# Optimization experiments

Hardware: AMD Instinct MI355X
Metric: run time of the kernel (lower is better)

Reference implementation:

```python
import jax, jax.numpy as jnp
import numpy as np

N_DRUG, N_DIS, E, D = 10000, 15000, 1048576, 128

def setup_inputs() -> dict:
    key = jax.random.key(0)
    k = jax.random.split(key, 6)
    return {
        "z_drug": jax.random.normal(k[0], (N_DRUG, D), dtype=jnp.float32),
        "z_disease": jax.random.normal(k[1], (N_DIS, D), dtype=jnp.float32),
        "row": jax.random.randint(k[2], (E,), 0, N_DRUG),
        "col": jax.random.randint(k[3], (E,), 0, N_DIS),
        "W1": jax.random.normal(k[4], (2 * D, D), dtype=jnp.float32) * (1.0 / np.sqrt(2 * D)),
        "b1": jnp.zeros((D,), dtype=jnp.float32),
        "W2": jax.random.normal(k[5], (D, 1), dtype=jnp.float32) * (1.0 / np.sqrt(D)),
        "b2": jnp.zeros((1,), dtype=jnp.float32),
    }

def reference(z_drug, z_disease, row, col, W1, b1, W2, b2):
    # gather per-edge embeddings and concatenate: [E, 2D]
    z = jnp.concatenate([z_drug[row], z_disease[col]], axis=-1)
    h = jax.nn.relu(z @ W1 + b1)          # [E, D]
    out = h @ W2 + b2                      # [E, 1]
    return out.reshape(-1)                 # [E]
```

## Files before the change

kernel.cpp:

```cpp
#include <hip/hip_runtime.h>

typedef __attribute__((ext_vector_type(8))) short short8;
typedef __attribute__((ext_vector_type(4))) float floatx4;
typedef _Float16 half8 __attribute__((ext_vector_type(8)));
typedef _Float16 half4 __attribute__((ext_vector_type(4)));
typedef _Float16 half2v __attribute__((ext_vector_type(2)));

static __device__ __forceinline__ unsigned short f2bf(float x) {
    unsigned int u = __builtin_bit_cast(unsigned int, x);
    unsigned int r = (u + 0x7FFFu + ((u >> 16) & 1u)) >> 16;
    return (unsigned short)r;
}

__global__ __launch_bounds__(256, 2) void mid_kernel(
    const float* __restrict__ zd, const float* __restrict__ zs,
    const float* __restrict__ W1, const float* __restrict__ b1,
    _Float16* __restrict__ ud, _Float16* __restrict__ us,
    int ndrows, int nsrows, int ntd, int nbg,
    const int* __restrict__ row, const int* __restrict__ col,
    unsigned* __restrict__ gcur, unsigned long long* __restrict__ recbuf, int E)
{
    if ((int)blockIdx.x < nbg) {
        const int tid  = threadIdx.x;
        const int lane = tid & 63;
        const int wave = tid >> 6;
        const int wh   = wave >> 1;
        const int we   = wave & 1;
        const int l15  = lane & 15;
        const int quad = lane >> 4;

        const int b = blockIdx.x;
        const bool isD = (b < ntd);
        const float* __restrict__ z = isD ? zd : zs;
        _Float16* __restrict__ u = isD ? ud : us;
        const int nrows = isD ? ndrows : nsrows;
        const int m0    = (isD ? b : b - ntd) * 64;
        const int koff0 = isD ? 0 : 128;
        const int whbase = wh * 64;

        short8 wfrag[16];
        #pragma unroll
        for (int s = 0; s < 4; ++s)
            #pragma unroll
            for (int mt = 0; mt < 4; ++mt) {
                short8 t;
                #pragma unroll
                for (int j = 0; j < 8; ++j)
                    t[j] = (short)f2bf(
                        W1[(size_t)(koff0 + s * 32 + quad * 8 + j) * 128 +
                           whbase + mt * 16 + l15]);
                wfrag[s * 4 + mt] = t;
            }

        floatx4 acc[2][4];
        #pragma unroll
        for (int mt = 0; mt < 4; ++mt) {
            floatx4 bb = *reinterpret_cast<const floatx4*>(&b1[whbase + mt * 16 + quad * 4]);
            bb *= 0.5f;
            acc[0][mt] = bb;
            acc[1][mt] = bb;
        }

        int rowi[2], rowc[2];
        #pragma unroll
        for (int et = 0; et < 2; ++et) {
            rowi[et] = m0 + we * 32 + et * 16 + l15;
            rowc[et] = rowi[et] < nrows ? rowi[et] : nrows - 1;
        }

        #pragma unroll
        for (int s = 0; s < 4; ++s) {
            short8 bf[2];
            #pragma unroll
            for (int et = 0; et < 2; ++et) {
                const float* src = &z[(size_t)rowc[et] * 128 + s * 32 + quad * 8];
                floatx4 lo = *reinterpret_cast<const floatx4*>(src);
                floatx4 hi = *reinterpret_cast<const floatx4*>(src + 4);
                short8 t;
                t[0] = (short)f2bf(lo[0]); t[1] = (short)f2bf(lo[1]);
                t[2] = (short)f2bf(lo[2]); t[3] = (short)f2bf(lo[3]);
                t[4] = (short)f2bf(hi[0]); t[5] = (short)f2bf(hi[1]);
                t[6] = (short)f2bf(hi[2]); t[7] = (short)f2bf(hi[3]);
                bf[et] = t;
            }
            #pragma unroll
            for (int et = 0; et < 2; ++et)
                #pragma unroll
                for (int mt = 0; mt < 4; ++mt)
                    acc[et][mt] = __builtin_amdgcn_mfma_f32_16x16x32_bf16(
                        wfrag[s * 4 + mt], bf[et], acc[et][mt], 0, 0, 0);
        }

        #pragma unroll
        for (int et = 0; et < 2; ++et) {
            if (rowi[et] < nrows) {
                #pragma unroll
                for (int mt = 0; mt < 4; ++mt) {
                    half4 hv;
                    #pragma unroll
                    for (int rr = 0; rr < 4; ++rr) hv[rr] = (_Float16)acc[et][mt][rr];
                    *reinterpret_cast<half4*>(
                        &u[(size_t)rowi[et] * 128 + whbase + mt * 16 + quad * 4]) = hv;
                }
            }
        }
    } else {
        __shared__ unsigned wl[4][4];
        __shared__ unsigned gb[4];
        const int tid  = threadIdx.x;
        const int lane = tid & 63;
        const int wave = tid >> 6;
        const int sb   = blockIdx.x - nbg;
        const long base = (long)sb * 2048;

        unsigned rc[8], off[8];
        int cls0, cls1, cls2, cls3, cls4, cls5, cls6, cls7;
        unsigned w0 = 0, w1 = 0, w2c = 0, w3 = 0;

        #pragma unroll
        for (int k = 0; k < 8; ++k) {
            long e = base + wave * 512 + k * 64 + lane;
            int r = row[e], c = col[e];
            rc[k] = (unsigned)r | ((unsigned)c << 14);
            int cl = ((r >= 5000) ? 2 : 0) | ((c >= 7500) ? 1 : 0);
            unsigned long long m0 = __ballot(cl == 0);
            unsigned long long m1 = __ballot(cl == 1);
            unsigned long long m2 = __ballot(cl == 2);
            unsigned long long m3 = __ballot(cl == 3);
            unsigned long long mlt = (1ull << lane) - 1ull;
            unsigned long long mc = (cl == 0) ? m0 : (cl == 1) ? m1 : (cl == 2) ? m2 : m3;
            unsigned wb = (cl == 0) ? w0 : (cl == 1) ? w1 : (cl == 2) ? w2c : w3;
            off[k] = wb + (unsigned)__popcll(mc & mlt);
            w0 += (unsigned)__popcll(m0); w1 += (unsigned)__popcll(m1);
            w2c += (unsigned)__popcll(m2); w3 += (unsigned)__popcll(m3);
            switch (k) {
                case 0: cls0 = cl; break; case 1: cls1 = cl; break;
                case 2: cls2 = cl; break; case 3: cls3 = cl; break;
                case 4: cls4 = cl; break; case 5: cls5 = cl; break;
                case 6: cls6 = cl; break; default: cls7 = cl; break;
            }
        }
        if (lane < 4) {
            unsigned wv = (lane == 0) ? w0 : (lane == 1) ? w1 : (lane == 2) ? w2c : w3;
            wl[wave][lane] = wv;
        }
        __syncthreads();
        if (tid < 4) {
            unsigned tot = wl[0][tid] + wl[1][tid] + wl[2][tid] + wl[3][tid];
            gb[tid] = atomicAdd(&gcur[tid], tot);
        }
        __syncthreads();
        unsigned p0 = 0, p1 = 0, p2 = 0, p3 = 0;
        for (int w = 0; w < 4; ++w)
            if (w < wave) { p0 += wl[w][0]; p1 += wl[w][1]; p2 += wl[w][2]; p3 += wl[w][3]; }

        #pragma unroll
        for (int k = 0; k < 8; ++k) {
            long e = base + wave * 512 + k * 64 + lane;
            int cl = (k == 0) ? cls0 : (k == 1) ? cls1 : (k == 2) ? cls2 : (k == 3) ? cls3
                   : (k == 4) ? cls4 : (k == 5) ? cls5 : (k == 6) ? cls6 : cls7;
            unsigned pre = (cl == 0) ? p0 : (cl == 1) ? p1 : (cl == 2) ? p2 : p3;
            unsigned pos = gb[cl] + pre + off[k];
            recbuf[(size_t)cl * E + pos] =
                (unsigned long long)rc[k] | ((unsigned long long)(unsigned)e << 32);
        }
    }
}

__global__ __launch_bounds__(256, 6) void edge_eval(
    const _Float16* __restrict__ ud, const _Float16* __restrict__ us,
    const unsigned* __restrict__ gcur, const unsigned long long* __restrict__ recbuf,
    const float* __restrict__ w2, const float* __restrict__ b2,
    float* __restrict__ out, int E)
{
    const int tid  = threadIdx.x;
    const int lane = tid & 63;
    const int wave = tid >> 6;
    const int le   = lane >> 3;
    const int q    = lane & 7;
    const int lslot = wave * 8 + le;

    const int b    = blockIdx.x;
    const int cls  = (b & 7) >> 1;
    const int sub  = ((b >> 3) << 1) | (b & 1);
    const int NSUB = (int)((gridDim.x >> 3) << 1);

    const unsigned n = gcur[cls];
    const int nch = (int)((n + 31u) >> 5);
    const unsigned long long* __restrict__ recb = recbuf + (size_t)cls * E;

#if __has_builtin(__builtin_amdgcn_fdot2)
    half2v w2h[8];
    #pragma unroll
    for (int i = 0; i < 2; ++i)
        #pragma unroll
        for (int p = 0; p < 4; ++p) {
            half2v t;
            t[0] = (_Float16)w2[i * 64 + q * 8 + 2 * p];
            t[1] = (_Float16)w2[i * 64 + q * 8 + 2 * p + 1];
            w2h[i * 4 + p] = t;
        }
#else
    float w2r[16];
    #pragma unroll
    for (int i = 0; i < 2; ++i) {
        *reinterpret_cast<floatx4*>(&w2r[i * 8]) =
            *reinterpret_cast<const floatx4*>(&w2[i * 64 + q * 8]);
        *reinterpret_cast<floatx4*>(&w2r[i * 8 + 4]) =
            *reinterpret_cast<const floatx4*>(&w2[i * 64 + q * 8 + 4]);
    }
#endif
    const float b2v = b2[0];

    const int K = (nch + NSUB - 1) / NSUB;
    int t = sub * K;
    int tend = t + K;
    if (tend > nch) tend = nch;
    if (t >= tend) return;

#define LOADREC(RV, VV, tt)                                                    \
    {                                                                          \
        unsigned ei = (unsigned)(tt) * 32u + (unsigned)lslot;                  \
        VV = ei < n;                                                           \
        RV = recb[VV ? ei : 0u];                                               \
    }

#define GATHER(D, RV)                                                          \
    {                                                                          \
        unsigned r = (unsigned)(RV) & 16383u;                                  \
        unsigned c = ((unsigned)(RV) >> 14) & 16383u;                          \
        const _Float16* up = ud + (size_t)r * 128 + q * 8;                     \
        const _Float16* vp = us + (size_t)c * 128 + q * 8;                     \
        D[0] = *reinterpret_cast<const half8*>(up);                            \
        D[1] = *reinterpret_cast<const half8*>(up + 64);                       \
        D[2] = *reinterpret_cast<const half8*>(vp);                            \
        D[3] = *reinterpret_cast<const half8*>(vp + 64);                       \
    }

#if __has_builtin(__builtin_amdgcn_fdot2)
#define DOTBODY(D, accv)                                                       \
    half8 s0 = D[0] + D[2];                                                    \
    s0 = __builtin_elementwise_max(s0, (half8)(_Float16)0.f);                  \
    half8 s1 = D[1] + D[3];                                                    \
    s1 = __builtin_elementwise_max(s1, (half8)(_Float16)0.f);                  \
    _Pragma("unroll")                                                          \
    for (int p = 0; p < 4; ++p) {                                              \
        half2v pr0; pr0[0] = s0[2 * p]; pr0[1] = s0[2 * p + 1];                \
        accv = __builtin_amdgcn_fdot2(pr0, w2h[p], accv, false);               \
        half2v pr1; pr1[0] = s1[2 * p]; pr1[1] = s1[2 * p + 1];                \
        accv = __builtin_amdgcn_fdot2(pr1, w2h[4 + p], accv, false);           \
    }
#else
#define DOTBODY(D, accv)                                                       \
    half8 s0 = D[0] + D[2];                                                    \
    s0 = __builtin_elementwise_max(s0, (half8)(_Float16)0.f);                  \
    half8 s1 = D[1] + D[3];                                                    \
    s1 = __builtin_elementwise_max(s1, (half8)(_Float16)0.f);                  \
    _Pragma("unroll")                                                          \
    for (int j = 0; j < 8; ++j) {                                              \
        accv += (float)s0[j] * w2r[j];                                         \
        accv += (float)s1[j] * w2r[8 + j];                                     \
    }
#endif

#define COMPUTE(D, RV, VV)                                                     \
    {                                                                          \
        float acc = 0.f;                                                       \
        DOTBODY(D, acc)                                                        \
        acc += __shfl_xor(acc, 1);                                             \
        acc += __shfl_xor(acc, 2);                                             \
        acc += __shfl_xor(acc, 4);                                             \
        if ((VV) && q == 0) out[(unsigned)((RV) >> 32)] = acc + b2v;           \
    }

    unsigned long long recA, recB = 0, recA2 = 0, recB2 = 0;
    bool vA, vB = false, vA2 = false, vB2 = false;
    LOADREC(recA, vA, t)
    bool hasB = (t + 1 < tend);
    if (hasB) LOADREC(recB, vB, t + 1)

    half8 dA[4], dB[4];
    while (true) {
        GATHER(dA, recA)
        if (hasB) GATHER(dB, recB)

        bool hasA2 = (t + 2 < tend), hasB2 = (t + 3 < tend);
        if (hasA2) LOADREC(recA2, vA2, t + 2)
        if (hasB2) LOADREC(recB2, vB2, t + 3)

        COMPUTE(dA, recA, vA)
        if (!hasB) break;
        COMPUTE(dB, recB, vB)

        if (!hasA2) break;
        recA = recA2; vA = vA2;
        recB = recB2; vB = vB2;
        hasB = hasB2;
        t += 2;
    }
#undef LOADREC
#undef GATHER
#undef DOTBODY
#undef COMPUTE
}

extern "C" void kernel_launch(void* const* d_in, const int* in_sizes, int n_in,
                              void* d_out, int out_size, void* d_ws, size_t ws_size,
                              hipStream_t stream) {
    const float* zd = (const float*)d_in[0];
    const float* zs = (const float*)d_in[1];
    const int*   row = (const int*)d_in[2];
    const int*   col = (const int*)d_in[3];
    const float* W1 = (const float*)d_in[4];
    const float* b1 = (const float*)d_in[5];
    const float* w2 = (const float*)d_in[6];
    const float* b2 = (const float*)d_in[7];
    float* out = (float*)d_out;

    const int nd = in_sizes[0];
    const int ns = in_sizes[1];
    const int E  = in_sizes[2];
    const int ndrows = nd / 128;
    const int nsrows = ns / 128;

    _Float16* ud = (_Float16*)d_ws;
    _Float16* us = ud + (size_t)ndrows * 128;
    size_t off = (size_t)((char*)(us + (size_t)nsrows * 128) - (char*)d_ws);
    off = (off + 63) & ~(size_t)63;
    unsigned* gcur = (unsigned*)((char*)d_ws + off);
    unsigned long long* recbuf = (unsigned long long*)((char*)gcur + 64);

    hipMemsetAsync(gcur, 0, 16 * sizeof(unsigned), stream);

    const int ntd = (ndrows + 63) / 64;
    const int nts = (nsrows + 63) / 64;
    const int nbg = ntd + nts;
    const int nsb = E / 2048;
    hipLaunchKernelGGL(mid_kernel, dim3(nbg + nsb), dim3(256), 0, stream,
                       zd, zs, W1, b1, ud, us, ndrows, nsrows, ntd, nbg,
                       row, col, gcur, recbuf, E);

    hipLaunchKernelGGL(edge_eval, dim3(1536), dim3(256), 0, stream,
                       ud, us, gcur, recbuf, w2, b2, out, E);
}
```

Before: 123.7 us.

## Replace 4-class edge partition with fine-grained row-bucket counting sort

The old code split edges into four coarse classes by row and column half. The new code builds a histogram over 16-row drug buckets crossed with two column halves, scans it, and scatters each record into a globally sorted order. Edges that share a drug row, or nearby rows, then sit next to each other, which should improve cache reuse of the gathered fp16 rows in the edge kernel. The cost is two more kernel launches (a single-block scan and a scatter pass), a second read of row and col, and local-memory atomics; the edge grid also drops from 1536 to 1024 blocks.

```diff
diff --git a/kernel.cpp b/kernel.cpp
--- a/kernel.cpp
+++ b/kernel.cpp
@@ -12,164 +12,207 @@
     return (unsigned short)r;
 }
 
-__global__ __launch_bounds__(256, 2) void mid_kernel(
+static __device__ void phase_gemm(
+    int b, const float* __restrict__ zd, const float* __restrict__ zs,
+    const float* __restrict__ W1, const float* __restrict__ b1,
+    _Float16* __restrict__ ud, _Float16* __restrict__ us,
+    int ndrows, int nsrows, int ntd)
+{
+    const int tid  = threadIdx.x;
+    const int lane = tid & 63;
+    const int wave = tid >> 6;
+    const int wh   = wave >> 1;
+    const int we   = wave & 1;
+    const int l15  = lane & 15;
+    const int quad = lane >> 4;
+
+    const bool isD = (b < ntd);
+    const float* __restrict__ z = isD ? zd : zs;
+    _Float16* __restrict__ u = isD ? ud : us;
+    const int nrows = isD ? ndrows : nsrows;
+    const int m0    = (isD ? b : b - ntd) * 64;
+    const int koff0 = isD ? 0 : 128;
+    const int whbase = wh * 64;
+
+    short8 wfrag[16];
+    #pragma unroll
+    for (int s = 0; s < 4; ++s)
+        #pragma unroll
+        for (int mt = 0; mt < 4; ++mt) {
+            short8 t;
+            #pragma unroll
+            for (int j = 0; j < 8; ++j)
+                t[j] = (short)f2bf(
+                    W1[(size_t)(koff0 + s * 32 + quad * 8 + j) * 128 +
+                       whbase + mt * 16 + l15]);
+            wfrag[s * 4 + mt] = t;
+        }
+
+    floatx4 acc[2][4];
+    #pragma unroll
+    for (int mt = 0; mt < 4; ++mt) {
+        floatx4 bb = *reinterpret_cast<const floatx4*>(&b1[whbase + mt * 16 + quad * 4]);
+        bb *= 0.5f;
+        acc[0][mt] = bb;
+        acc[1][mt] = bb;
+    }
+
+    int rowi[2], rowc[2];
+    #pragma unroll
+    for (int et = 0; et < 2; ++et) {
+        rowi[et] = m0 + we * 32 + et * 16 + l15;
+        rowc[et] = rowi[et] < nrows ? rowi[et] : nrows - 1;
+    }
+
+    #pragma unroll
+    for (int s = 0; s < 4; ++s) {
+        short8 bf[2];
+        #pragma unroll
+        for (int et = 0; et < 2; ++et) {
+            const float* src = &z[(size_t)rowc[et] * 128 + s * 32 + quad * 8];
+            floatx4 lo = *reinterpret_cast<const floatx4*>(src);
+            floatx4 hi = *reinterpret_cast<const floatx4*>(src + 4);
+            short8 t;
+            t[0] = (short)f2bf(lo[0]); t[1] = (short)f2bf(lo[1]);
+            t[2] = (short)f2bf(lo[2]); t[3] = (short)f2bf(lo[3]);
+            t[4] = (short)f2bf(hi[0]); t[5] = (short)f2bf(hi[1]);
+            t[6] = (short)f2bf(hi[2]); t[7] = (short)f2bf(hi[3]);
+            bf[et] = t;
+        }
+        #pragma unroll
+        for (int et = 0; et < 2; ++et)
+            #pragma unroll
+            for (int mt = 0; mt < 4; ++mt)
+                acc[et][mt] = __builtin_amdgcn_mfma_f32_16x16x32_bf16(
+                    wfrag[s * 4 + mt], bf[et], acc[et][mt], 0, 0, 0);
+    }
+
+    #pragma unroll
+    for (int et = 0; et < 2; ++et) {
+        if (rowi[et] < nrows) {
+            #pragma unroll
+            for (int mt = 0; mt < 4; ++mt) {
+                half4 hv;
+                #pragma unroll
+                for (int rr = 0; rr < 4; ++rr) hv[rr] = (_Float16)acc[et][mt][rr];
+                *reinterpret_cast<half4*>(
+                    &u[(size_t)rowi[et] * 128 + whbase + mt * 16 + quad * 4]) = hv;
+            }
+        }
+    }
+}
+
+static __device__ void phase_hist(
+    int hb, const int* __restrict__ row, const int* __restrict__ col,
+    unsigned* __restrict__ ghist, int E, int nbrow, int colh)
+{
+    __shared__ unsigned lh[1280];
+    const int tid = threadIdx.x;
+    for (int i = tid; i < 1280; i += 256) lh[i] = 0;
+    __syncthreads();
+    const int per = (E + 191) / 192;
+    const int e0 = hb * per;
+    int e1 = e0 + per; if (e1 > E) e1 = E;
+    for (int e = e0 + tid; e < e1; e += 256) {
+        int r = row[e], c = col[e];
+        int bin = ((c >= colh) ? nbrow : 0) + (r >> 4);
+        atomicAdd(&lh[bin], 1u);
+    }
+    __syncthreads();
+    const int nb = 2 * nbrow;
+    for (int i = tid; i < nb; i += 256) {
+        unsigned v = lh[i];
+        if (v) atomicAdd(&ghist[i], v);
+    }
+}
+
+__global__ __launch_bounds__(256, 2) void k_mid(
     const float* __restrict__ zd, const float* __restrict__ zs,
     const float* __restrict__ W1, const float* __restrict__ b1,
     _Float16* __restrict__ ud, _Float16* __restrict__ us,
     int ndrows, int nsrows, int ntd, int nbg,
     const int* __restrict__ row, const int* __restrict__ col,
-    unsigned* __restrict__ gcur, unsigned long long* __restrict__ recbuf, int E)
-{
-    if ((int)blockIdx.x < nbg) {
-        const int tid  = threadIdx.x;
-        const int lane = tid & 63;
-        const int wave = tid >> 6;
-        const int wh   = wave >> 1;
-        const int we   = wave & 1;
-        const int l15  = lane & 15;
-        const int quad = lane >> 4;
-
-        const int b = blockIdx.x;
-        const bool isD = (b < ntd);
-        const float* __restrict__ z = isD ? zd : zs;
-        _Float16* __restrict__ u = isD ? ud : us;
-        const int nrows = isD ? ndrows : nsrows;
-        const int m0    = (isD ? b : b - ntd) * 64;
-        const int koff0 = isD ? 0 : 128;
-        const int whbase = wh * 64;
-
-        short8 wfrag[16];
-        #pragma unroll
-        for (int s = 0; s < 4; ++s)
-            #pragma unroll
-            for (int mt = 0; mt < 4; ++mt) {
-                short8 t;
-                #pragma unroll
-                for (int j = 0; j < 8; ++j)
-                    t[j] = (short)f2bf(
-                        W1[(size_t)(koff0 + s * 32 + quad * 8 + j) * 128 +
-                           whbase + mt * 16 + l15]);
-                wfrag[s * 4 + mt] = t;
-            }
-
-        floatx4 acc[2][4];
-        #pragma unroll
-        for (int mt = 0; mt < 4; ++mt) {
-            floatx4 bb = *reinterpret_cast<const floatx4*>(&b1[whbase + mt * 16 + quad * 4]);
-            bb *= 0.5f;
-            acc[0][mt] = bb;
-            acc[1][mt] = bb;
+    unsigned* __restrict__ ghist, int E, int nbrow, int colh)
+{
+    const int b = blockIdx.x;
+    if (b < nbg) phase_gemm(b, zd, zs, W1, b1, ud, us, ndrows, nsrows, ntd);
+    else         phase_hist(b - nbg, row, col, ghist, E, nbrow, colh);
+}
+
+__global__ void k_scan(const unsigned* __restrict__ ghist, unsigned* __restrict__ gcur,
+                       unsigned* __restrict__ gmeta, int nb, int nbrow)
+{
+    __shared__ unsigned tsum[256];
+    const int tid = threadIdx.x;
+    unsigned v[5];
+    unsigned s = 0;
+    #pragma unroll
+    for (int i = 0; i < 5; ++i) {
+        int idx = tid * 5 + i;
+        v[i] = (idx < nb) ? ghist[idx] : 0u;
+        s += v[i];
+    }
+    tsum[tid] = s;
+    for (int off = 1; off < 256; off <<= 1) {
+        __syncthreads();
+        unsigned y = (tid >= off) ? tsum[tid - off] : 0u;
+        __syncthreads();
+        tsum[tid] += y;
+    }
+    __syncthreads();
+    unsigned running = tsum[tid] - s;
+    #pragma unroll
+    for (int i = 0; i < 5; ++i) {
+        int idx = tid * 5 + i;
+        if (idx < nb) {
+            gcur[idx] = running;
+            if (idx == nbrow) gmeta[0] = running;
+            running += v[i];
         }
-
-        int rowi[2], rowc[2];
-        #pragma unroll
-        for (int et = 0; et < 2; ++et) {
-            rowi[et] = m0 + we * 32 + et * 16 + l15;
-            rowc[et] = rowi[et] < nrows ? rowi[et] : nrows - 1;
-        }
-
-        #pragma unroll
-        for (int s = 0; s < 4; ++s) {
-            short8 bf[2];
-            #pragma unroll
-            for (int et = 0; et < 2; ++et) {
-                const float* src = &z[(size_t)rowc[et] * 128 + s * 32 + quad * 8];
-                floatx4 lo = *reinterpret_cast<const floatx4*>(src);
-                floatx4 hi = *reinterpret_cast<const floatx4*>(src + 4);
-                short8 t;
-                t[0] = (short)f2bf(lo[0]); t[1] = (short)f2bf(lo[1]);
-                t[2] = (short)f2bf(lo[2]); t[3] = (short)f2bf(lo[3]);
-                t[4] = (short)f2bf(hi[0]); t[5] = (short)f2bf(hi[1]);
-                t[6] = (short)f2bf(hi[2]); t[7] = (short)f2bf(hi[3]);
-                bf[et] = t;
-            }
-            #pragma unroll
-            for (int et = 0; et < 2; ++et)
-                #pragma unroll
-                for (int mt = 0; mt < 4; ++mt)
-                    acc[et][mt] = __builtin_amdgcn_mfma_f32_16x16x32_bf16(
-                        wfrag[s * 4 + mt], bf[et], acc[et][mt], 0, 0, 0);
-        }
-
-        #pragma unroll
-        for (int et = 0; et < 2; ++et) {
-            if (rowi[et] < nrows) {
-                #pragma unroll
-                for (int mt = 0; mt < 4; ++mt) {
-                    half4 hv;
-                    #pragma unroll
-                    for (int rr = 0; rr < 4; ++rr) hv[rr] = (_Float16)acc[et][mt][rr];
-                    *reinterpret_cast<half4*>(
-                        &u[(size_t)rowi[et] * 128 + whbase + mt * 16 + quad * 4]) = hv;
-                }
-            }
-        }
-    } else {
-        __shared__ unsigned wl[4][4];
-        __shared__ unsigned gb[4];
-        const int tid  = threadIdx.x;
-        const int lane = tid & 63;
-        const int wave = tid >> 6;
-        const int sb   = blockIdx.x - nbg;
-        const long base = (long)sb * 2048;
-
-        unsigned rc[8], off[8];
-        int cls0, cls1, cls2, cls3, cls4, cls5, cls6, cls7;
-        unsigned w0 = 0, w1 = 0, w2c = 0, w3 = 0;
-
-        #pragma unroll
-        for (int k = 0; k < 8; ++k) {
-            long e = base + wave * 512 + k * 64 + lane;
-            int r = row[e], c = col[e];
-            rc[k] = (unsigned)r | ((unsigned)c << 14);
-            int cl = ((r >= 5000) ? 2 : 0) | ((c >= 7500) ? 1 : 0);
-            unsigned long long m0 = __ballot(cl == 0);
-            unsigned long long m1 = __ballot(cl == 1);
-            unsigned long long m2 = __ballot(cl == 2);
-            unsigned long long m3 = __ballot(cl == 3);
-            unsigned long long mlt = (1ull << lane) - 1ull;
-            unsigned long long mc = (cl == 0) ? m0 : (cl == 1) ? m1 : (cl == 2) ? m2 : m3;
-            unsigned wb = (cl == 0) ? w0 : (cl == 1) ? w1 : (cl == 2) ? w2c : w3;
-            off[k] = wb + (unsigned)__popcll(mc & mlt);
-            w0 += (unsigned)__popcll(m0); w1 += (unsigned)__popcll(m1);
-            w2c += (unsigned)__popcll(m2); w3 += (unsigned)__popcll(m3);
-            switch (k) {
-                case 0: cls0 = cl; break; case 1: cls1 = cl; break;
-                case 2: cls2 = cl; break; case 3: cls3 = cl; break;
-                case 4: cls4 = cl; break; case 5: cls5 = cl; break;
-                case 6: cls6 = cl; break; default: cls7 = cl; break;
-            }
-        }
-        if (lane < 4) {
-            unsigned wv = (lane == 0) ? w0 : (lane == 1) ? w1 : (lane == 2) ? w2c : w3;
-            wl[wave][lane] = wv;
-        }
-        __syncthreads();
-        if (tid < 4) {
-            unsigned tot = wl[0][tid] + wl[1][tid] + wl[2][tid] + wl[3][tid];
-            gb[tid] = atomicAdd(&gcur[tid], tot);
-        }
-        __syncthreads();
-        unsigned p0 = 0, p1 = 0, p2 = 0, p3 = 0;
-        for (int w = 0; w < 4; ++w)
-            if (w < wave) { p0 += wl[w][0]; p1 += wl[w][1]; p2 += wl[w][2]; p3 += wl[w][3]; }
-
-        #pragma unroll
-        for (int k = 0; k < 8; ++k) {
-            long e = base + wave * 512 + k * 64 + lane;
-            int cl = (k == 0) ? cls0 : (k == 1) ? cls1 : (k == 2) ? cls2 : (k == 3) ? cls3
-                   : (k == 4) ? cls4 : (k == 5) ? cls5 : (k == 6) ? cls6 : cls7;
-            unsigned pre = (cl == 0) ? p0 : (cl == 1) ? p1 : (cl == 2) ? p2 : p3;
-            unsigned pos = gb[cl] + pre + off[k];
-            recbuf[(size_t)cl * E + pos] =
-                (unsigned long long)rc[k] | ((unsigned long long)(unsigned)e << 32);
-        }
-    }
-}
-
-__global__ __launch_bounds__(256, 6) void edge_eval(
+    }
+}
+
+__global__ __launch_bounds__(256, 4) void k_scatter(
+    const int* __restrict__ row, const int* __restrict__ col,
+    unsigned* __restrict__ gcur, unsigned long long* __restrict__ recbuf,
+    int E, int nbrow, int colh)
+{
+    __shared__ unsigned lh[1280];
+    const int tid = threadIdx.x;
+    for (int i = tid; i < 1280; i += 256) lh[i] = 0;
+    __syncthreads();
+
+    const int per = E >> 9;
+    const long base = (long)blockIdx.x * per;
+
+    unsigned rnk[8], rcv[8];
+    int binv[8];
+    #pragma unroll
+    for (int k = 0; k < 8; ++k) {
+        long e = base + k * 256 + tid;
+        int r = row[e], c = col[e];
+        rcv[k] = (unsigned)r | ((unsigned)c << 14);
+        binv[k] = ((c >= colh) ? nbrow : 0) + (r >> 4);
+        rnk[k] = atomicAdd(&lh[binv[k]], 1u);
+    }
+    __syncthreads();
+    const int nb = 2 * nbrow;
+    for (int i = tid; i < nb; i += 256) {
+        unsigned cnt = lh[i];
+        if (cnt) lh[i] = atomicAdd(&gcur[i], cnt);
+    }
+    __syncthreads();
+    #pragma unroll
+    for (int k = 0; k < 8; ++k) {
+        long e = base + k * 256 + tid;
+        unsigned pos = lh[binv[k]] + rnk[k];
+        recbuf[pos] = (unsigned long long)rcv[k] | ((unsigned long long)(unsigned)e << 32);
+    }
+}
+
+__global__ __launch_bounds__(256, 4) void k_edge(
     const _Float16* __restrict__ ud, const _Float16* __restrict__ us,
-    const unsigned* __restrict__ gcur, const unsigned long long* __restrict__ recbuf,
+    const unsigned* __restrict__ gmeta, const unsigned long long* __restrict__ recbuf,
     const float* __restrict__ w2, const float* __restrict__ b2,
     float* __restrict__ out, int E)
 {
@@ -180,14 +223,19 @@
     const int q    = lane & 7;
     const int lslot = wave * 8 + le;
 
-    const int b    = blockIdx.x;
-    const int cls  = (b & 7) >> 1;
-    const int sub  = ((b >> 3) << 1) | (b & 1);
-    const int NSUB = (int)((gridDim.x >> 3) << 1);
-
-    const unsigned n = gcur[cls];
-    const int nch = (int)((n + 31u) >> 5);
-    const unsigned long long* __restrict__ recb = recbuf + (size_t)cls * E;
+    const int b   = blockIdx.x;
+    const int cc  = (b & 7) >> 2;
+    const int sub = ((b >> 3) << 2) | (b & 3);
+    const unsigned n0 = gmeta[0];
+    const unsigned c0 = cc ? n0 : 0u;
+    const unsigned nc = cc ? ((unsigned)E - n0) : n0;
+    if (nc == 0) return;
+    const unsigned K = (nc + 511u) >> 9;
+    unsigned start = c0 + (unsigned)sub * K;
+    unsigned climit = c0 + nc;
+    if (start >= climit) return;
+    unsigned end = start + K;
+    if (end > climit) end = climit;
 
 #if __has_builtin(__builtin_amdgcn_fdot2)
     half2v w2h[8];
@@ -211,18 +259,13 @@
     }
 #endif
     const float b2v = b2[0];
-
-    const int K = (nch + NSUB - 1) / NSUB;
-    int t = sub * K;
-    int tend = t + K;
-    if (tend > nch) tend = nch;
-    if (t >= tend) return;
+    const int tend = (int)((end - start + 31u) >> 5);
 
 #define LOADREC(RV, VV, tt)                                                    \
     {                                                                          \
-        unsigned ei = (unsigned)(tt) * 32u + (unsigned)lslot;                  \
-        VV = ei < n;                                                           \
-        RV = recb[VV ? ei : 0u];                                               \
+        unsigned ei = start + (unsigned)(tt) * 32u + (unsigned)lslot;          \
+        VV = ei < end;                                                         \
+        RV = recbuf[VV ? ei : start];                                          \
     }
 
 #define GATHER(D, RV)                                                          \
@@ -275,9 +318,10 @@
 
     unsigned long long recA, recB = 0, recA2 = 0, recB2 = 0;
     bool vA, vB = false, vA2 = false, vB2 = false;
-    LOADREC(recA, vA, t)
-    bool hasB = (t + 1 < tend);
-    if (hasB) LOADREC(recB, vB, t + 1)
+    int t = 0;
+    LOADREC(recA, vA, 0)
+    bool hasB = (1 < tend);
+    if (hasB) LOADREC(recB, vB, 1)
 
     half8 dA[4], dB[4];
     while (true) {
@@ -322,24 +366,35 @@
     const int E  = in_sizes[2];
     const int ndrows = nd / 128;
     const int nsrows = ns / 128;
+    const int nbrow = (ndrows + 15) >> 4;
+    const int nb = 2 * nbrow;
+    const int colh = nsrows >> 1;
 
     _Float16* ud = (_Float16*)d_ws;
     _Float16* us = ud + (size_t)ndrows * 128;
     size_t off = (size_t)((char*)(us + (size_t)nsrows * 128) - (char*)d_ws);
     off = (off + 63) & ~(size_t)63;
-    unsigned* gcur = (unsigned*)((char*)d_ws + off);
-    unsigned long long* recbuf = (unsigned long long*)((char*)gcur + 64);
-
-    hipMemsetAsync(gcur, 0, 16 * sizeof(unsigned), stream);
+    unsigned* gmeta = (unsigned*)((char*)d_ws + off);
+    unsigned* ghist = gmeta + 16;
+    unsigned* gcur  = ghist + 1280;
+    unsigned long long* recbuf =
+        (unsigned long long*)(((uintptr_t)(gcur + 1280) + 63) & ~(uintptr_t)63);
+
+    hipMemsetAsync(gmeta, 0, (16 + 1280) * sizeof(unsigned), stream);
 
     const int ntd = (ndrows + 63) / 64;
     const int nts = (nsrows + 63) / 64;
     const int nbg = ntd + nts;
-    const int nsb = E / 2048;
-    hipLaunchKernelGGL(mid_kernel, dim3(nbg + nsb), dim3(256), 0, stream,
+    hipLaunchKernelGGL(k_mid, dim3(nbg + 192), dim3(256), 0, stream,
                        zd, zs, W1, b1, ud, us, ndrows, nsrows, ntd, nbg,
-                       row, col, gcur, recbuf, E);
-
-    hipLaunchKernelGGL(edge_eval, dim3(1536), dim3(256), 0, stream,
-                       ud, us, gcur, recbuf, w2, b2, out, E);
-}
+                       row, col, ghist, E, nbrow, colh);
+
+    hipLaunchKernelGGL(k_scan, dim3(1), dim3(256), 0, stream,
+                       ghist, gcur, gmeta, nb, nbrow);
+
+    hipLaunchKernelGGL(k_scatter, dim3(512), dim3(256), 0, stream,
+                       row, col, gcur, recbuf, E, nbrow, colh);
+
+    hipLaunchKernelGGL(k_edge, dim3(1024), dim3(256), 0, stream,
+                       ud, us, gmeta, recbuf, w2, b2, out, E);
+}
```

New measurement: 152.3 us. 23.2% more time.
